# Optimization experiments

Measured on AMD Instinct MI355X. Metric: run time of the kernel, lower is better.

## Reference

```python
import jax, jax.numpy as jnp
import numpy as np

NEG_INF = -1e5  # module default neg_inf


def setup_inputs() -> dict:
    key = jax.random.key(0)
    k1, k2 = jax.random.split(key)
    B, T, V, U = 64, 1000, 512, 256
    log_posteriors = jax.random.normal(k1, (B, T, V), dtype=jnp.float32)
    lens = jnp.ones((B,), dtype=jnp.float32)
    phns = jax.random.randint(k2, (B, U), 0, V)
    phn_lens = jnp.ones((B,), dtype=jnp.float32)
    return {"log_posteriors": log_posteriors, "lens": lens, "phns": phns, "phn_lens": phn_lens}


def _forward_scores(log_posteriors, lens, phns, phn_lens):
    B, T, V = log_posteriors.shape
    U = phns.shape[1]
    lens_abs = jnp.round(lens * T).astype(jnp.int32)
    phn_lens_abs = jnp.round(phn_lens * U).astype(jnp.int32)

    # --- pi: all initial mass on first phoneme ---
    pi = jnp.full((B, U), NEG_INF, dtype=jnp.float32).at[:, 0].set(0.0)

    # --- transition log-probs: self-loop + advance-by-one, length-masked, row log_softmax ---
    base = jnp.eye(U, dtype=jnp.float32) + jnp.eye(U, k=1, dtype=jnp.float32)  # (U,U)
    m = jnp.arange(U)[None, :] < phn_lens_abs[:, None]  # (B,U) valid-phoneme mask
    m2 = m[:, :, None] & m[:, None, :]  # (B,U,U)
    masked = base[None, :, :] * m2.astype(jnp.float32)
    logits = jnp.where(masked == 1.0, 1.0, -jnp.inf)
    trans = jax.nn.log_softmax(logits, axis=2)
    # nan (all -inf rows) and -inf -> neg_inf, as in the torch module
    trans = jnp.where(jnp.isnan(trans) | jnp.isinf(trans), NEG_INF, trans)  # (B,U,U)

    # --- emissions rearranged to phoneme-sequence order: (B, U, T) as (T, B, U) scan seq ---
    mask_t = jnp.arange(T)[None, :] < lens_abs[:, None]  # (B,T)
    ep = jnp.where(mask_t[:, :, None], log_posteriors, NEG_INF)
    idx = jnp.broadcast_to(phns[:, None, :], (B, T, U))
    gathered = jnp.take_along_axis(ep, idx, axis=2)  # (B,T,U)
    emiss = jnp.where(m[:, None, :], gathered, NEG_INF)  # (B,T,U)
    emiss_seq = jnp.swapaxes(emiss, 0, 1)  # (T,B,U)

    # --- forward DP: alpha[t,i] = logsumexp_j(trans[j,i] + alpha[t-1,j]) + emiss[t,i] ---
    transT = jnp.swapaxes(trans, 1, 2)  # (B, to, from)
    alpha0 = pi + emiss_seq[0]  # (B,U), unmasked as in torch (masked entries ~2*neg_inf anyway)

    def step(alpha, e_t):
        x = jax.nn.logsumexp(transT + alpha[:, None, :], axis=2)  # batch_log_matvecmul
        alpha_new = jnp.where(m, x + e_t, NEG_INF)
        return alpha_new, None

    alphaT, _ = jax.lax.scan(step, alpha0, emiss_seq[1:])
    return jax.nn.logsumexp(alphaT, axis=1)  # (B,) log-likelihoods


def reference(log_posteriors, lens, phns, phn_lens):
    return _forward_scores(log_posteriors, lens, phns, phn_lens)
```

## Files before the change

### kernel.cpp

```cpp
#include <hip/hip_runtime.h>
#include <math.h>

constexpr int Bc = 64;
constexpr int Tc = 1000;
constexpr int Vc = 512;
constexpr int Uc = 256;
constexpr int CH = 50;
constexpr int NCH = Tc / CH;
constexpr int PW = 7;
constexpr int SLOTS = 4;

constexpr int GW = 2;
constexpr int GNR = 10;
constexpr int GROWS = GW * GNR;
constexpr int GBLK = Tc / GROWS;

constexpr int FPC = CH * Uc * 2 / 1024;

#define NEG_INF_F (-100000.0f)
#define LOG2E_F 1.44269504088896340736f
#define LN2_F 0.69314718055994530942f
#define DEAD_F (-1.0e9f)
#define EBIAS 30

#define WAITVM(n) __builtin_amdgcn_s_waitcnt(((n) & 15) | (((n) >> 4) << 14) | 0x0f70)

__device__ __forceinline__ float fexp2(float x) {
#if __has_builtin(__builtin_amdgcn_exp2f)
    return __builtin_amdgcn_exp2f(x);
#else
    return __expf(x * LN2_F);
#endif
}
__device__ __forceinline__ float flog2(float x) {
#if __has_builtin(__builtin_amdgcn_logf)
    return __builtin_amdgcn_logf(x);
#else
    return __logf(x) * LOG2E_F;
#endif
}

__device__ __forceinline__ float l2add(float x, float y) {
    float m = fmaxf(x, y);
    float p = fexp2(-fabsf(x - y));
    return m + flog2(1.0f + p);
}

__device__ __forceinline__ float waveshr1(float x, float lane0val) {
    return __int_as_float(__builtin_amdgcn_update_dpp(
        __float_as_int(lane0val), __float_as_int(x),
        0x138 , 0xF, 0xF, false));
}
__device__ __forceinline__ int waveshr1_i(int x) {
    return __builtin_amdgcn_update_dpp(x, x, 0x138, 0xF, 0xF, false);
}

__device__ __forceinline__ float4 unbf(uint2 u) {
    float4 f;
    f.x = __uint_as_float(u.x << 16);
    f.y = __uint_as_float(u.x & 0xffff0000u);
    f.z = __uint_as_float(u.y << 16);
    f.w = __uint_as_float(u.y & 0xffff0000u);
    return f;
}
__device__ __forceinline__ unsigned int bfpack(float a, float b) {
    unsigned int xa = __float_as_uint(a), xb = __float_as_uint(b);
    xa = (xa + 0x7fffu + ((xa >> 16) & 1u)) >> 16;
    xb = (xb + 0x7fffu + ((xb >> 16) & 1u)) & 0xffff0000u;
    return xa | xb;
}

__device__ __forceinline__ void hmm_step_f32(float rr[4], const float4 ev,
                                             float sc_d) {
    float nb0 = waveshr1(rr[3], 0.0f) * sc_d;
    float s0 = rr[0] + nb0;
    float s1 = rr[1] + rr[0];
    float s2 = rr[2] + rr[1];
    float s3 = rr[3] + rr[2];
    rr[0] = s0 * ev.x;
    rr[1] = s1 * ev.y;
    rr[2] = s2 * ev.z;
    rr[3] = s3 * ev.w;
}

__device__ __forceinline__ void hmm_step(float rr[4], const float4 ev) {
    float nb0 = waveshr1(rr[3], DEAD_F);
    float e[4] = {ev.x, ev.y, ev.z, ev.w};
    float nb[4] = {nb0, rr[0], rr[1], rr[2]};
#pragma unroll
    for (int c = 0; c < 4; ++c) {
        float x = rr[c], y = nb[c];
        float m = fmaxf(x, y);
        float p = fexp2(-fabsf(x - y));
        float me = m + e[c];
        rr[c] = me + flog2(1.0f + p);
    }
}

template <int AUX>
__device__ __forceinline__ void dma16x(const void* gsrc, void* lds, int lane) {
    typedef const __attribute__((address_space(1))) unsigned int* gp_t;
    typedef __attribute__((address_space(3))) unsigned int* lp_t;
    __builtin_amdgcn_global_load_lds((gp_t)((const char*)gsrc + 16 * lane),
                                     (lp_t)lds, 16, 0, AUX);
}
__device__ __forceinline__ void dma16(const void* g, void* l, int lane) {
    dma16x<0>(g, l, lane);
}
__device__ __forceinline__ void dma16nt(const void* g, void* l, int lane) {
    dma16x<2>(g, l, lane);
}

__global__ __launch_bounds__(128, 2) void gather_kernel(
    const float* __restrict__ lp, const float* __restrict__ lens,
    const int* __restrict__ phns, const float* __restrict__ phn_lens,
    unsigned short* __restrict__ el) {
    __shared__ float stage[GW][GNR][Vc];
    const int b = blockIdx.x;
    const int t0 = blockIdx.y * GROWS;
    const int tid = threadIdx.x;
    const int wave = tid >> 6;
    const int lane = tid & 63;
    const int Tv = (int)rintf(lens[b] * (float)Tc);
    const int Uv = (int)rintf(phn_lens[b] * (float)Uc);
    const float* lpb = lp + (size_t)b * Tc * Vc;
    unsigned short* elb = el + ((size_t)b * Tc + t0) * Uc;

    int col[4];
    float off[4];
    bool pv[4];
    int4 cc = *(const int4*)(phns + (size_t)b * Uc + 4 * lane);
    int c4[4] = {cc.x, cc.y, cc.z, cc.w};
#pragma unroll
    for (int c = 0; c < 4; ++c) {
        int v = c4[c];
        v = v < 0 ? 0 : (v > Vc - 1 ? Vc - 1 : v);
        col[c] = v;
        int i = 4 * lane + c;
        pv[c] = (i < Uv);
        off[c] = (i == Uv - 1) ? 0.0f : -1.0f;
    }

    float* stw = &stage[wave][0][0];
#pragma unroll
    for (int j = 0; j < GNR; ++j) {
        int r = wave + j * GW;
        const float* gsrc = lpb + (size_t)(t0 + r) * Vc;
        float* st = stw + j * Vc;
        dma16nt(gsrc, st, lane);
        dma16nt(gsrc + 256, st + 256, lane);
    }

    auto do_rows = [&](int j0) {
#pragma unroll
        for (int j = j0; j < j0 + GNR / 2; ++j) {
            int r = wave + j * GW;
            const bool tv = (t0 + r) < Tv;
            const float* st = stw + j * Vc;
            float ev[4];
#pragma unroll
            for (int c = 0; c < 4; ++c) {
                float e = st[col[c]];
                ev[c] = (pv[c] && tv) ? fexp2(fmaf(e, LOG2E_F, off[c])) : 0.0f;
            }
            uint2 pk;
            pk.x = bfpack(ev[0], ev[1]);
            pk.y = bfpack(ev[2], ev[3]);
            *(uint2*)((char*)elb + (size_t)r * Uc * 2 + 8 * lane) = pk;
        }
    };

    WAITVM(10);
    do_rows(0);
    WAITVM(0);
    do_rows(GNR / 2);
}

__global__ __launch_bounds__(64, 1) void scan_kernel(
    const unsigned short* __restrict__ el, const float* __restrict__ phn_lens,
    float* __restrict__ out) {
    __shared__ unsigned short ebuf[3][CH][Uc];
    const int b = blockIdx.x;
    const int lane = threadIdx.x & 63;
    const int Uv = (int)rintf(phn_lens[b] * (float)Uc);
    const char* eb = (const char*)(el + (size_t)b * Tc * Uc);
    float rr[4];
    int e = 0;
    float sc_d = 1.0f;

    auto fill = [&](int k) {
        const char* src = eb + (size_t)k * CH * Uc * 2;
        char* dst = (char*)&ebuf[k % 3][0][0];
#pragma unroll
        for (int i = 0; i < FPC; ++i)
            dma16(src + i * 1024, dst + i * 1024, lane);
    };

    auto renorm = [&]() {
        float m = fmaxf(fmaxf(rr[0], rr[1]), fmaxf(rr[2], rr[3]));
        int ep_old = waveshr1_i(e);
        bool nz = (m > 0.0f);
        int ik = ((__float_as_int(m) >> 23) & 255) - 127 - EBIAS;
        ik = ik < -96 ? -96 : (ik > 96 ? 96 : ik);
        const float sc = __int_as_float((127 - ik) << 23);
        rr[0] *= sc; rr[1] *= sc; rr[2] *= sc; rr[3] *= sc;
        e = nz ? (e + ik) : ep_old;
        int ep = waveshr1_i(e);
        int d = ep - e;
        int dc = d < -126 ? -126 : (d > 127 ? 127 : d);
        float sd = __int_as_float((127 + dc) << 23);
        sc_d = (d < -126) ? 0.0f : sd;
    };

    auto consume = [&](int k) {
        const uint2* base = (const uint2*)&ebuf[k % 3][0][0] + lane;
        int r = 0;
        if (k == 0) {
            float4 e0 = unbf(base[0]);
            float ea[4] = {e0.x, e0.y, e0.z, e0.w};
#pragma unroll
            for (int c = 0; c < 4; ++c)
                rr[c] = (4 * lane + c == 0) ? ea[c] : 0.0f;
            r = 1;
        }
        uint2 q0, q1, q2, q3;
        if (r + 0 < CH) q0 = base[(r + 0) * 64];
        if (r + 1 < CH) q1 = base[(r + 1) * 64];
        if (r + 2 < CH) q2 = base[(r + 2) * 64];
        if (r + 3 < CH) q3 = base[(r + 3) * 64];
        while (r + 4 <= CH) {
            uint2 e0 = q0, e1 = q1, e2v = q2, e3 = q3;
            if (r + 4 < CH) q0 = base[(r + 4) * 64];
            if (r + 5 < CH) q1 = base[(r + 5) * 64];
            if (r + 6 < CH) q2 = base[(r + 6) * 64];
            if (r + 7 < CH) q3 = base[(r + 7) * 64];
            hmm_step_f32(rr, unbf(e0), sc_d);
            hmm_step_f32(rr, unbf(e1), sc_d);
            hmm_step_f32(rr, unbf(e2v), sc_d);
            hmm_step_f32(rr, unbf(e3), sc_d);
            renorm();
            r += 4;
        }
        bool tail = false;
        if (r + 0 < CH) { hmm_step_f32(rr, unbf(q0), sc_d); tail = true; }
        if (r + 1 < CH) { hmm_step_f32(rr, unbf(q1), sc_d); }
        if (r + 2 < CH) { hmm_step_f32(rr, unbf(q2), sc_d); }
        if (tail) renorm();
    };

    WAITVM(0);
    fill(0);
    fill(1);
    fill(2);
    for (int k = 0; k < NCH; ++k) {
        if (k + 2 < NCH) WAITVM(2 * FPC);
        else if (k + 1 < NCH) WAITVM(FPC);
        else WAITVM(0);
        consume(k);
        if (k + 3 < NCH) fill(k + 3);
    }

    float a = 0.0f;
#pragma unroll
    for (int c = 0; c < 4; ++c)
        a += rr[c] * ((4 * lane + c == Uv - 1) ? 1.0f : 2.0f);
    float v = (a > 0.0f) ? (flog2(a) + (float)e) : -1.0e30f;
#pragma unroll
    for (int o = 32; o >= 1; o >>= 1) {
        float t = __shfl_xor(v, o, 64);
        v = l2add(v, t);
    }
    if (lane == 0) out[b] = v * LN2_F;
}

__global__ __launch_bounds__(512, 1) void fused_hmm_kernel(
    const float* __restrict__ lp, const float* __restrict__ lens,
    const int* __restrict__ phns, const float* __restrict__ phn_lens,
    float* __restrict__ out) {
    __shared__ float ebuf[2][CH][Uc];
    __shared__ float stage[PW][SLOTS][Vc];
    const int b = blockIdx.x;
    const int tid = threadIdx.x;
    const int wave = tid >> 6;
    const int lane = tid & 63;
    const int Tv = (int)rintf(lens[b] * (float)Tc);
    const int Uv = (int)rintf(phn_lens[b] * (float)Uc);
    const float* lpb = lp + (size_t)b * Tc * Vc;

    int col[4];
    float off[4];
    bool pv[4];
    float rr[4];

    if (wave > 0) {
        int4 cc = *(const int4*)(phns + (size_t)b * Uc + 4 * lane);
        int c4[4] = {cc.x, cc.y, cc.z, cc.w};
#pragma unroll
        for (int c = 0; c < 4; ++c) {
            int v = c4[c];
            v = v < 0 ? 0 : (v > Vc - 1 ? Vc - 1 : v);
            col[c] = v;
            int i = 4 * lane + c;
            pv[c] = (i < Uv);
            off[c] = (i == Uv - 1) ? 0.0f : -1.0f;
        }
    }

    auto fill = [&](int k) {
        float* dst = &ebuf[k & 1][0][0];
        const int tb = k * CH;
        const int r0 = wave - 1;
        float* stw = &stage[wave - 1][0][0];
#pragma unroll
        for (int half = 0; half < 2; ++half) {
#pragma unroll
            for (int jj = 0; jj < SLOTS; ++jj) {
                int r = r0 + (half * SLOTS + jj) * PW;
                if (r < CH) {
                    const float* gsrc = lpb + (size_t)(tb + r) * Vc;
                    float* st = stw + jj * Vc;
                    dma16(gsrc, st, lane);
                    dma16(gsrc + 256, st + 256, lane);
                }
            }
            WAITVM(0);
#pragma unroll
            for (int jj = 0; jj < SLOTS; ++jj) {
                int r = r0 + (half * SLOTS + jj) * PW;
                if (r < CH) {
                    const bool tv = (tb + r) < Tv;
                    const float* st = stw + jj * Vc;
                    float ev[4];
#pragma unroll
                    for (int c = 0; c < 4; ++c) {
                        float e = st[col[c]];
                        ev[c] = (pv[c] && tv) ? fmaf(e, LOG2E_F, off[c])
                                              : (NEG_INF_F * LOG2E_F + off[c]);
                    }
                    *(float4*)(dst + r * Uc + 4 * lane) =
                        make_float4(ev[0], ev[1], ev[2], ev[3]);
                }
            }
        }
    };

    auto consume = [&](int k) {
        const float4* base = (const float4*)&ebuf[k & 1][0][0] + lane;
        int r = 0;
        if (k == 0) {
            float4 e0 = base[0];
            float ea[4] = {e0.x, e0.y, e0.z, e0.w};
#pragma unroll
            for (int c = 0; c < 4; ++c)
                rr[c] = ((4 * lane + c == 0) ? 0.0f : DEAD_F) + ea[c];
            r = 1;
        }
        float4 q0, q1, q2, q3;
        if (r + 0 < CH) q0 = base[(r + 0) * 64];
        if (r + 1 < CH) q1 = base[(r + 1) * 64];
        if (r + 2 < CH) q2 = base[(r + 2) * 64];
        if (r + 3 < CH) q3 = base[(r + 3) * 64];
        while (r + 4 <= CH) {
            float4 e0 = q0, e1 = q1, e2 = q2, e3 = q3;
            if (r + 4 < CH) q0 = base[(r + 4) * 64];
            if (r + 5 < CH) q1 = base[(r + 5) * 64];
            if (r + 6 < CH) q2 = base[(r + 6) * 64];
            if (r + 7 < CH) q3 = base[(r + 7) * 64];
            hmm_step(rr, e0);
            hmm_step(rr, e1);
            hmm_step(rr, e2);
            hmm_step(rr, e3);
            r += 4;
        }
        if (r + 0 < CH) hmm_step(rr, q0);
        if (r + 1 < CH) hmm_step(rr, q1);
        if (r + 2 < CH) hmm_step(rr, q2);
    };

    if (wave > 0) fill(0);
    __syncthreads();
    for (int k = 0; k < NCH; ++k) {
        if (wave > 0) {
            if (k + 1 < NCH) fill(k + 1);
        } else {
            consume(k);
        }
        __syncthreads();
    }

    if (wave == 0) {
        float a[4];
#pragma unroll
        for (int c = 0; c < 4; ++c)
            a[c] = rr[c] + ((4 * lane + c == Uv - 1) ? 0.0f : 1.0f);
        float r2 = l2add(l2add(a[0], a[1]), l2add(a[2], a[3]));
#pragma unroll
        for (int o = 32; o >= 1; o >>= 1) {
            float t = __shfl_xor(r2, o, 64);
            r2 = l2add(r2, t);
        }
        if (lane == 0) out[b] = r2 * LN2_F;
    }
}

extern "C" void kernel_launch(void* const* d_in, const int* in_sizes, int n_in,
                              void* d_out, int out_size, void* d_ws, size_t ws_size,
                              hipStream_t stream) {
    const float* lp = (const float*)d_in[0];
    const float* lens = (const float*)d_in[1];
    const int* phns = (const int*)d_in[2];
    const float* phn_lens = (const float*)d_in[3];
    float* out = (float*)d_out;
    (void)in_sizes; (void)n_in; (void)out_size;

    const size_t need = (size_t)Bc * Tc * Uc * 2;
    if (d_ws != nullptr && ws_size >= need) {
        unsigned short* el = (unsigned short*)d_ws;
        gather_kernel<<<dim3(Bc, GBLK), 128, 0, stream>>>(lp, lens, phns,
                                                          phn_lens, el);
        scan_kernel<<<Bc, 64, 0, stream>>>(el, phn_lens, out);
    } else {
        fused_hmm_kernel<<<Bc, 512, 0, stream>>>(lp, lens, phns, phn_lens, out);
    }
}
```

Measured before the change: 245.9 us.

## Split scan prefetch across two waves with four-slot LDS ring buffer

The scan kernel now launches two waves per batch. Wave 0 runs the serial HMM recurrence, and the two waves take turns issuing the async DMA fills for even and odd chunks. The LDS ring grows from three to four slots. Handoff for the odd chunks uses two __syncthreads per odd chunk. This takes some of the load-issue and wait work off the critical compute wave, at the cost of block-wide barriers on the serial path.

```diff
diff --git a/kernel.cpp b/kernel.cpp
--- a/kernel.cpp
+++ b/kernel.cpp
@@ -176,12 +176,14 @@
     do_rows(GNR / 2);
 }
 
-__global__ __launch_bounds__(64, 1) void scan_kernel(
+__global__ __launch_bounds__(128, 1) void scan_kernel(
     const unsigned short* __restrict__ el, const float* __restrict__ phn_lens,
     float* __restrict__ out) {
-    __shared__ unsigned short ebuf[3][CH][Uc];
+    __shared__ unsigned short ebuf[4][CH][Uc];
     const int b = blockIdx.x;
-    const int lane = threadIdx.x & 63;
+    const int tid = threadIdx.x;
+    const int wave = tid >> 6;
+    const int lane = tid & 63;
     const int Uv = (int)rintf(phn_lens[b] * (float)Uc);
     const char* eb = (const char*)(el + (size_t)b * Tc * Uc);
     float rr[4];
@@ -190,7 +192,7 @@
 
     auto fill = [&](int k) {
         const char* src = eb + (size_t)k * CH * Uc * 2;
-        char* dst = (char*)&ebuf[k % 3][0][0];
+        char* dst = (char*)&ebuf[k & 3][0][0];
 #pragma unroll
         for (int i = 0; i < FPC; ++i)
             dma16(src + i * 1024, dst + i * 1024, lane);
@@ -213,7 +215,7 @@
     };
 
     auto consume = [&](int k) {
-        const uint2* base = (const uint2*)&ebuf[k % 3][0][0] + lane;
+        const uint2* base = (const uint2*)&ebuf[k & 3][0][0] + lane;
         int r = 0;
         if (k == 0) {
             float4 e0 = unbf(base[0]);
@@ -249,17 +251,33 @@
     };
 
     WAITVM(0);
-    fill(0);
-    fill(1);
-    fill(2);
+    if (wave == 0) {
+        fill(0); fill(2);
+    } else {
+        fill(1); fill(3);
+    }
+
     for (int k = 0; k < NCH; ++k) {
-        if (k + 2 < NCH) WAITVM(2 * FPC);
-        else if (k + 1 < NCH) WAITVM(FPC);
-        else WAITVM(0);
-        consume(k);
-        if (k + 3 < NCH) fill(k + 3);
-    }
-
+        if ((k & 1) == 0) {
+            if (wave == 0) {
+                if (k < NCH - 2) WAITVM(FPC);
+                else WAITVM(0);
+                consume(k);
+                if (k + 4 < NCH) fill(k + 4);
+            }
+        } else {
+            if (wave == 1) {
+                if (k < NCH - 2) WAITVM(FPC);
+                else WAITVM(0);
+            }
+            __syncthreads();
+            if (wave == 0) consume(k);
+            __syncthreads();
+            if (wave == 1 && k + 4 < NCH) fill(k + 4);
+        }
+    }
+
+    if (wave != 0) return;
     float a = 0.0f;
 #pragma unroll
     for (int c = 0; c < 4; ++c)
@@ -418,7 +436,7 @@
         unsigned short* el = (unsigned short*)d_ws;
         gather_kernel<<<dim3(Bc, GBLK), 128, 0, stream>>>(lp, lens, phns,
                                                           phn_lens, el);
-        scan_kernel<<<Bc, 64, 0, stream>>>(el, phn_lens, out);
+        scan_kernel<<<Bc, 128, 0, stream>>>(el, phn_lens, out);
     } else {
         fused_hmm_kernel<<<Bc, 512, 0, stream>>>(lp, lens, phns, phn_lens, out);
     }
```

Measured after the change: 241.0 us. 2.0% less time.
